# Kernel optimization log

Measured on AMD Instinct MI355X. Metric: run time of the kernel, lower is better.

## Reference

```python
import jax, jax.numpy as jnp
import numpy as np

B, S, W = 64, 128, 20
VOCAB, E, H = 256, 64, 256


def setup_inputs() -> dict:
    key = jax.random.key(0)
    ks = jax.random.split(key, 10)
    return {
        "chars": jax.random.randint(ks[0], (B, S, W), 0, VOCAB),
        "emb": jax.random.uniform(ks[1], (VOCAB, E), jnp.float32, -0.32, 0.32),
        "w1": jax.random.normal(ks[2], (H, E, 1), jnp.float32) * 0.1,
        "b1": jax.random.normal(ks[3], (H,), jnp.float32) * 0.1,
        "w3": jax.random.normal(ks[4], (H, E, 3), jnp.float32) * 0.1,
        "b3": jax.random.normal(ks[5], (H,), jnp.float32) * 0.1,
        "w5": jax.random.normal(ks[6], (H, E, 5), jnp.float32) * 0.1,
        "b5": jax.random.normal(ks[7], (H,), jnp.float32) * 0.1,
        "lw": jax.random.normal(ks[8], (H, 3 * H), jnp.float32) * 0.05,
        "lb": jax.random.normal(ks[9], (H,), jnp.float32) * 0.05,
    }


def _conv_relu_maxpool(x, w, b):
    # x: [N, E, W], w: [H, E, k] ('same' padding k//2) -> [N, H]
    k = w.shape[-1]
    pad = k // 2
    y = jax.lax.conv_general_dilated(
        x, w, window_strides=(1,), padding=[(pad, pad)],
        dimension_numbers=("NCH", "OIH", "NCH"))
    y = jax.nn.relu(y + b[None, :, None])
    return jnp.max(y, axis=2)  # global max over char positions


def reference(chars, emb, w1, b1, w3, b3, w5, b5, lw, lb):
    b, s, wlen = chars.shape
    flat = chars.reshape(-1, wlen)                 # [N, W]
    x = emb[flat]                                  # [N, W, E]
    x = jnp.transpose(x, (0, 2, 1))                # [N, E, W]
    outs = jnp.concatenate([
        _conv_relu_maxpool(x, w1, b1),
        _conv_relu_maxpool(x, w3, b3),
        _conv_relu_maxpool(x, w5, b5),
    ], axis=1)                                     # [N, 3H]
    out = outs @ lw.T + lb                         # [N, H]
    return out.reshape(b, s, -1)
```

## Files before the change

kernel.cpp:

```cpp
#include <hip/hip_runtime.h>
#include <hip/hip_bf16.h>

#define WW 20
#define NW 8192
#define VOCAB 256
#define EE 64
#define HH 256
#define K3 768
#define NTAP 9
#define UNIT 2304

typedef short bf16x8 __attribute__((ext_vector_type(8)));
typedef float f32x4  __attribute__((ext_vector_type(4)));

__device__ __forceinline__ ushort f2bs(float x) {
    __hip_bfloat16 h = __float2bfloat16(x);
    union { __hip_bfloat16 h; ushort u; } c; c.h = h; return c.u;
}
__device__ __forceinline__ float blo(unsigned u) {
    union { unsigned i; float f; } c; c.i = u << 16; return c.f;
}
__device__ __forceinline__ float bhi(unsigned u) {
    union { unsigned i; float f; } c; c.i = u & 0xffff0000u; return c.f;
}
__device__ __forceinline__ unsigned pack2(float lo, float hi) {
    return (unsigned)f2bs(lo) | ((unsigned)f2bs(hi) << 16);
}

#define SET2(d, w) { d[0] = blo(w); d[1] = bhi(w); }
#define ADD2(d, w) { d[0] += blo(w); d[1] += bhi(w); }
#define MAX2(m, s) { m[0] = fmaxf(m[0], s[0]); m[1] = fmaxf(m[1], s[1]); }


__global__ __launch_bounds__(256) void prep(
        const float* __restrict__ w1,
        const float* __restrict__ w3,
        const float* __restrict__ w5,
        const float* __restrict__ lw,
        float* __restrict__ wTp,
        ushort* __restrict__ lwb) {
    const int bid = blockIdx.x;
    if (bid < 576) {
        int idx = bid * 256 + threadIdx.x;
        int e = idx / UNIT;
        int j = idx - e * UNIT;
        int o  = j / 1152;
        int jh = j - o * 1152;
        int tap, h;
        if (jh < 1024) {
            int c = jh >> 8, q = jh & 255, u = q >> 2, p = q & 3;
            tap = 2*c + (p >> 1);
            h   = o*128 + 2*u + (p & 1);
        } else { tap = 8; h = o*128 + (jh - 1024); }
        float v;
        if (tap == 0)      v = w1[h*EE + e];
        else if (tap <= 3) v = w3[(h*EE + e)*3 + (tap-1)];
        else               v = w5[(h*EE + e)*5 + (tap-4)];
        wTp[idx] = v;
    } else {
        int i = ((bid - 576) * 256 + threadIdx.x) * 4;
        float4 v = *(const float4*)(lw + i);
        ushort4 o4;
        o4.x = f2bs(v.x); o4.y = f2bs(v.y); o4.z = f2bs(v.z); o4.w = f2bs(v.w);
        *(ushort4*)(lwb + i) = o4;
    }
}

__global__ __launch_bounds__(256) void build_tables(
        const float* __restrict__ emb,
        const float* __restrict__ wTp,
        ushort* __restrict__ P3) {
    __shared__ float emb_s[4][EE];
    const int v0 = blockIdx.x * 4;
    const int j  = blockIdx.y * 256 + threadIdx.x;
    const int t  = threadIdx.x;
    emb_s[t >> 6][t & 63] = emb[v0*EE + t];
    __syncthreads();

    float a0 = 0.f, a1 = 0.f, a2 = 0.f, a3 = 0.f;
    const float* wp = wTp + j;
    #pragma unroll 8
    for (int e = 0; e < EE; ++e) {
        float w = wp[e * UNIT];
        a0 += emb_s[0][e] * w; a1 += emb_s[1][e] * w;
        a2 += emb_s[2][e] * w; a3 += emb_s[3][e] * w;
    }
    P3[(size_t)(v0+0)*UNIT + j] = f2bs(a0);
    P3[(size_t)(v0+1)*UNIT + j] = f2bs(a1);
    P3[(size_t)(v0+2)*UNIT + j] = f2bs(a2);
    P3[(size_t)(v0+3)*UNIT + j] = f2bs(a3);
}

__global__ __launch_bounds__(256) void conv_pool(
        const int* __restrict__ chars,
        const ushort* __restrict__ P3,
        const float* __restrict__ b1,
        const float* __restrict__ b3,
        const float* __restrict__ b5,
        ushort* __restrict__ outs) {
    const int tid  = threadIdx.x;
    const int wave = tid >> 6, lane = tid & 63;
    const int n    = blockIdx.x * 2 + (wave >> 1);
    const int o    = wave & 1;

    int cv = chars[n * WW + (lane < WW ? lane : WW - 1)];
    int c[WW];
    #pragma unroll
    for (int j = 0; j < WW; ++j) c[j] = __builtin_amdgcn_readlane(cv, j);

    const ushort* base = P3 + o * 1152;

    float acc3[3][2], acc5[5][2], m1[2], m3[2], m5[2];
    acc3[0][0]=0.f; acc3[0][1]=0.f;
    acc5[0][0]=0.f; acc5[0][1]=0.f; acc5[1][0]=0.f; acc5[1][1]=0.f;
    m1[0]=-1e30f; m1[1]=-1e30f; m3[0]=-1e30f; m3[1]=-1e30f;
    m5[0]=-1e30f; m5[1]=-1e30f;

    uint2 q[2][4]; unsigned t8[2];
    {
        const ushort* p = base + (size_t)c[0] * UNIT;
        #pragma unroll
        for (int i = 0; i < 4; ++i) q[0][i] = *(const uint2*)(p + i*256 + lane*4);
        t8[0] = *(const unsigned*)(p + 1024 + lane*2);
    }

    #pragma unroll
    for (int j = 0; j < WW; ++j) {
        const int cur = j & 1, nxt = cur ^ 1;
        if (j + 1 < WW) {
            const ushort* p = base + (size_t)c[j+1] * UNIT;
            #pragma unroll
            for (int i = 0; i < 4; ++i) q[nxt][i] = *(const uint2*)(p + i*256 + lane*4);
            t8[nxt] = *(const unsigned*)(p + 1024 + lane*2);
        }
        uint2 q0 = q[cur][0], q1 = q[cur][1], q2 = q[cur][2], q3 = q[cur][3];
        unsigned e8 = t8[cur];

        m1[0] = fmaxf(m1[0], blo(q0.x)); m1[1] = fmaxf(m1[1], bhi(q0.x));
        if (j + 1 < WW) SET2(acc3[(j+1)%3], q0.y)
        ADD2(acc3[j%3], q1.x)
        if (j >= 1) { ADD2(acc3[(j-1)%3], q1.y)
                      MAX2(m3, acc3[(j-1)%3]) }
        if (j + 2 < WW) SET2(acc5[(j+2)%5], q2.x)
        if (j + 1 < WW) ADD2(acc5[(j+1)%5], q2.y)
        ADD2(acc5[j%5], q3.x)
        if (j >= 1) ADD2(acc5[(j-1)%5], q3.y)
        if (j >= 2) { ADD2(acc5[(j-2)%5], e8)
                      MAX2(m5, acc5[(j-2)%5]) }
    }
    MAX2(m3, acc3[(WW-1)%3])
    MAX2(m5, acc5[(WW-2)%5])
    MAX2(m5, acc5[(WW-1)%5])

    const int h0 = o*128 + lane*2;
    float2 bb1 = *(const float2*)(b1 + h0);
    float2 bb3 = *(const float2*)(b3 + h0);
    float2 bb5 = *(const float2*)(b5 + h0);
    unsigned* op = (unsigned*)(outs + (size_t)n * K3 + h0);
    op[0*(HH/2)] = pack2(fmaxf(m1[0]+bb1.x, 0.f), fmaxf(m1[1]+bb1.y, 0.f));
    op[1*(HH/2)] = pack2(fmaxf(m3[0]+bb3.x, 0.f), fmaxf(m3[1]+bb3.y, 0.f));
    op[2*(HH/2)] = pack2(fmaxf(m5[0]+bb5.x, 0.f), fmaxf(m5[1]+bb5.y, 0.f));
}

__global__ __launch_bounds__(64) void gemm_out(
        const ushort* __restrict__ outs,
        const ushort* __restrict__ lwb,
        const float* __restrict__ lb,
        float* __restrict__ out) {
    const int lane = threadIdx.x;
    const int m0 = blockIdx.x * 16;
    const int n0 = blockIdx.y * 32;
    const int mrow = lane & 15, quad = lane >> 4;

    f32x4 acc0 = (f32x4){0,0,0,0}, acc1 = (f32x4){0,0,0,0};
    const ushort* ap = outs + (size_t)(m0 + mrow) * K3 + quad * 8;
    const ushort* bp = lwb  + (size_t)(n0 + mrow) * K3 + quad * 8;

    bf16x8 a  = *(const bf16x8*)ap;
    bf16x8 b0 = *(const bf16x8*)bp;
    bf16x8 b1 = *(const bf16x8*)(bp + 16*K3);

    #pragma unroll
    for (int it = 0; it < K3/32; ++it) {
        const int kn = (it + 1 < K3/32) ? (it + 1) * 32 : 0;
        bf16x8 an  = *(const bf16x8*)(ap + kn);
        bf16x8 b0n = *(const bf16x8*)(bp + kn);
        bf16x8 b1n = *(const bf16x8*)(bp + 16*K3 + kn);
        acc0 = __builtin_amdgcn_mfma_f32_16x16x32_bf16(a, b0, acc0, 0, 0, 0);
        acc1 = __builtin_amdgcn_mfma_f32_16x16x32_bf16(a, b1, acc1, 0, 0, 0);
        a = an; b0 = b0n; b1 = b1n;
    }

    #pragma unroll
    for (int nn = 0; nn < 2; ++nn) {
        const f32x4 acc = nn ? acc1 : acc0;
        int ncol = n0 + nn*16 + mrow;
        float lbv = lb[ncol];
        #pragma unroll
        for (int r = 0; r < 4; ++r)
            out[(size_t)(m0 + quad*4 + r)*HH + ncol] = acc[r] + lbv;
    }
}

extern "C" void kernel_launch(void* const* d_in, const int* in_sizes, int n_in,
                              void* d_out, int out_size, void* d_ws, size_t ws_size,
                              hipStream_t stream) {
    const int*   chars = (const int*)d_in[0];
    const float* emb   = (const float*)d_in[1];
    const float* w1    = (const float*)d_in[2];
    const float* b1    = (const float*)d_in[3];
    const float* w3    = (const float*)d_in[4];
    const float* b3    = (const float*)d_in[5];
    const float* w5    = (const float*)d_in[6];
    const float* b5    = (const float*)d_in[7];
    const float* lw    = (const float*)d_in[8];
    const float* lb    = (const float*)d_in[9];

    ushort* P3   = (ushort*)d_ws;
    float*  wTp  = (float*)(P3 + VOCAB * UNIT);
    ushort* outs = (ushort*)(wTp + EE * UNIT);
    ushort* lwb  = outs + (size_t)NW * K3;

    prep<<<768, 256, 0, stream>>>(w1, w3, w5, lw, wTp, lwb);
    build_tables<<<dim3(VOCAB/4, NTAP), 256, 0, stream>>>(emb, wTp, P3);
    conv_pool<<<NW/2, 256, 0, stream>>>(chars, P3, b1, b3, b5, outs);
    gemm_out<<<dim3(NW/16, HH/32), 64, 0, stream>>>(outs, lwb, lb, (float*)d_out);
}
```

Before: 161.4 us.

## Repack per-vocab tap table to per-channel contiguous 10-tap layout

The precomputed embedding-times-weight table is reorganised so that each output channel's nine taps sit contiguously, padded to ten entries, per vocab entry. The conv_pool kernel then does one 16-byte and one 4-byte load per character per thread instead of five scattered loads, and handles one channel per thread with one word per block. Lanes now read 20-byte strided addresses, which may coalesce less well. The table grows from nine to ten taps per channel and the output stores become 2-byte writes.

```diff
diff --git a/kernel.cpp b/kernel.cpp
--- a/kernel.cpp
+++ b/kernel.cpp
@@ -7,8 +7,7 @@
 #define EE 64
 #define HH 256
 #define K3 768
-#define NTAP 9
-#define UNIT 2304
+#define UNIT4 2560
 
 typedef short bf16x8 __attribute__((ext_vector_type(8)));
 typedef float f32x4  __attribute__((ext_vector_type(4)));
@@ -23,13 +22,6 @@
 __device__ __forceinline__ float bhi(unsigned u) {
     union { unsigned i; float f; } c; c.i = u & 0xffff0000u; return c.f;
 }
-__device__ __forceinline__ unsigned pack2(float lo, float hi) {
-    return (unsigned)f2bs(lo) | ((unsigned)f2bs(hi) << 16);
-}
-
-#define SET2(d, w) { d[0] = blo(w); d[1] = bhi(w); }
-#define ADD2(d, w) { d[0] += blo(w); d[1] += bhi(w); }
-#define MAX2(m, s) { m[0] = fmaxf(m[0], s[0]); m[1] = fmaxf(m[1], s[1]); }
 
 
 __global__ __launch_bounds__(256) void prep(
@@ -40,25 +32,19 @@
         float* __restrict__ wTp,
         ushort* __restrict__ lwb) {
     const int bid = blockIdx.x;
-    if (bid < 576) {
+    if (bid < 640) {
         int idx = bid * 256 + threadIdx.x;
-        int e = idx / UNIT;
-        int j = idx - e * UNIT;
-        int o  = j / 1152;
-        int jh = j - o * 1152;
-        int tap, h;
-        if (jh < 1024) {
-            int c = jh >> 8, q = jh & 255, u = q >> 2, p = q & 3;
-            tap = 2*c + (p >> 1);
-            h   = o*128 + 2*u + (p & 1);
-        } else { tap = 8; h = o*128 + (jh - 1024); }
-        float v;
+        int e = idx / UNIT4;
+        int j = idx - e * UNIT4;
+        int h = j / 10;
+        int tap = j - h * 10;
+        float v = 0.f;
         if (tap == 0)      v = w1[h*EE + e];
         else if (tap <= 3) v = w3[(h*EE + e)*3 + (tap-1)];
-        else               v = w5[(h*EE + e)*5 + (tap-4)];
+        else if (tap <= 8) v = w5[(h*EE + e)*5 + (tap-4)];
         wTp[idx] = v;
     } else {
-        int i = ((bid - 576) * 256 + threadIdx.x) * 4;
+        int i = ((bid - 640) * 256 + threadIdx.x) * 4;
         float4 v = *(const float4*)(lw + i);
         ushort4 o4;
         o4.x = f2bs(v.x); o4.y = f2bs(v.y); o4.z = f2bs(v.z); o4.w = f2bs(v.w);
@@ -69,7 +55,7 @@
 __global__ __launch_bounds__(256) void build_tables(
         const float* __restrict__ emb,
         const float* __restrict__ wTp,
-        ushort* __restrict__ P3) {
+        ushort* __restrict__ P4) {
     __shared__ float emb_s[4][EE];
     const int v0 = blockIdx.x * 4;
     const int j  = blockIdx.y * 256 + threadIdx.x;
@@ -81,85 +67,81 @@
     const float* wp = wTp + j;
     #pragma unroll 8
     for (int e = 0; e < EE; ++e) {
-        float w = wp[e * UNIT];
+        float w = wp[e * UNIT4];
         a0 += emb_s[0][e] * w; a1 += emb_s[1][e] * w;
         a2 += emb_s[2][e] * w; a3 += emb_s[3][e] * w;
     }
-    P3[(size_t)(v0+0)*UNIT + j] = f2bs(a0);
-    P3[(size_t)(v0+1)*UNIT + j] = f2bs(a1);
-    P3[(size_t)(v0+2)*UNIT + j] = f2bs(a2);
-    P3[(size_t)(v0+3)*UNIT + j] = f2bs(a3);
+    P4[(size_t)(v0+0)*UNIT4 + j] = f2bs(a0);
+    P4[(size_t)(v0+1)*UNIT4 + j] = f2bs(a1);
+    P4[(size_t)(v0+2)*UNIT4 + j] = f2bs(a2);
+    P4[(size_t)(v0+3)*UNIT4 + j] = f2bs(a3);
 }
 
 __global__ __launch_bounds__(256) void conv_pool(
         const int* __restrict__ chars,
-        const ushort* __restrict__ P3,
+        const ushort* __restrict__ P4,
         const float* __restrict__ b1,
         const float* __restrict__ b3,
         const float* __restrict__ b5,
         ushort* __restrict__ outs) {
     const int tid  = threadIdx.x;
     const int wave = tid >> 6, lane = tid & 63;
-    const int n    = blockIdx.x * 2 + (wave >> 1);
-    const int o    = wave & 1;
+    const int n    = blockIdx.x;
+    const int h    = wave * 64 + lane;
+    const int hb   = h * 20;
 
     int cv = chars[n * WW + (lane < WW ? lane : WW - 1)];
     int c[WW];
     #pragma unroll
     for (int j = 0; j < WW; ++j) c[j] = __builtin_amdgcn_readlane(cv, j);
 
-    const ushort* base = P3 + o * 1152;
-
-    float acc3[3][2], acc5[5][2], m1[2], m3[2], m5[2];
-    acc3[0][0]=0.f; acc3[0][1]=0.f;
-    acc5[0][0]=0.f; acc5[0][1]=0.f; acc5[1][0]=0.f; acc5[1][1]=0.f;
-    m1[0]=-1e30f; m1[1]=-1e30f; m3[0]=-1e30f; m3[1]=-1e30f;
-    m5[0]=-1e30f; m5[1]=-1e30f;
-
-    uint2 q[2][4]; unsigned t8[2];
+    float acc3[3], acc5[5], m1, m3, m5;
+    acc3[0] = 0.f; acc5[0] = 0.f; acc5[1] = 0.f;
+    m1 = -1e30f; m3 = -1e30f; m5 = -1e30f;
+
+    uint4 q[2]; unsigned t8[2];
     {
-        const ushort* p = base + (size_t)c[0] * UNIT;
-        #pragma unroll
-        for (int i = 0; i < 4; ++i) q[0][i] = *(const uint2*)(p + i*256 + lane*4);
-        t8[0] = *(const unsigned*)(p + 1024 + lane*2);
+        const char* p = (const char*)P4 + (size_t)c[0] * 5120;
+        q[0]  = *(const uint4*)(p + hb);
+        t8[0] = *(const unsigned*)(p + hb + 16);
     }
 
     #pragma unroll
     for (int j = 0; j < WW; ++j) {
         const int cur = j & 1, nxt = cur ^ 1;
         if (j + 1 < WW) {
-            const ushort* p = base + (size_t)c[j+1] * UNIT;
-            #pragma unroll
-            for (int i = 0; i < 4; ++i) q[nxt][i] = *(const uint2*)(p + i*256 + lane*4);
-            t8[nxt] = *(const unsigned*)(p + 1024 + lane*2);
+            const char* p = (const char*)P4 + (size_t)c[j+1] * 5120;
+            q[nxt]  = *(const uint4*)(p + hb);
+            t8[nxt] = *(const unsigned*)(p + hb + 16);
         }
-        uint2 q0 = q[cur][0], q1 = q[cur][1], q2 = q[cur][2], q3 = q[cur][3];
-        unsigned e8 = t8[cur];
-
-        m1[0] = fmaxf(m1[0], blo(q0.x)); m1[1] = fmaxf(m1[1], bhi(q0.x));
-        if (j + 1 < WW) SET2(acc3[(j+1)%3], q0.y)
-        ADD2(acc3[j%3], q1.x)
-        if (j >= 1) { ADD2(acc3[(j-1)%3], q1.y)
-                      MAX2(m3, acc3[(j-1)%3]) }
-        if (j + 2 < WW) SET2(acc5[(j+2)%5], q2.x)
-        if (j + 1 < WW) ADD2(acc5[(j+1)%5], q2.y)
-        ADD2(acc5[j%5], q3.x)
-        if (j >= 1) ADD2(acc5[(j-1)%5], q3.y)
-        if (j >= 2) { ADD2(acc5[(j-2)%5], e8)
-                      MAX2(m5, acc5[(j-2)%5]) }
-    }
-    MAX2(m3, acc3[(WW-1)%3])
-    MAX2(m5, acc5[(WW-2)%5])
-    MAX2(m5, acc5[(WW-1)%5])
-
-    const int h0 = o*128 + lane*2;
-    float2 bb1 = *(const float2*)(b1 + h0);
-    float2 bb3 = *(const float2*)(b3 + h0);
-    float2 bb5 = *(const float2*)(b5 + h0);
-    unsigned* op = (unsigned*)(outs + (size_t)n * K3 + h0);
-    op[0*(HH/2)] = pack2(fmaxf(m1[0]+bb1.x, 0.f), fmaxf(m1[1]+bb1.y, 0.f));
-    op[1*(HH/2)] = pack2(fmaxf(m3[0]+bb3.x, 0.f), fmaxf(m3[1]+bb3.y, 0.f));
-    op[2*(HH/2)] = pack2(fmaxf(m5[0]+bb5.x, 0.f), fmaxf(m5[1]+bb5.y, 0.f));
+        uint4 qq = q[cur];
+        float t0 = blo(qq.x), t1 = bhi(qq.x), t2 = blo(qq.y), t3 = bhi(qq.y);
+        float t4 = blo(qq.z), t5 = bhi(qq.z), t6 = blo(qq.w), t7 = bhi(qq.w);
+        float t8v = blo(t8[cur]);
+
+        m1 = fmaxf(m1, t0);
+        if (j + 1 < WW) acc3[(j+1)%3] = t1;
+        acc3[j%3] += t2;
+        if (j >= 1) { acc3[(j-1)%3] += t3;
+                      m3 = fmaxf(m3, acc3[(j-1)%3]); }
+        if (j + 2 < WW) acc5[(j+2)%5] = t4;
+        if (j + 1 < WW) acc5[(j+1)%5] += t5;
+        acc5[j%5] += t6;
+        if (j >= 1) acc5[(j-1)%5] += t7;
+        if (j >= 2) { acc5[(j-2)%5] += t8v;
+                      m5 = fmaxf(m5, acc5[(j-2)%5]); }
+    }
+    m3 = fmaxf(m3, acc3[(WW-1)%3]);
+    m5 = fmaxf(m5, acc5[(WW-2)%5]);
+    m5 = fmaxf(m5, acc5[(WW-1)%5]);
+
+    float v1 = fmaxf(m1 + b1[h], 0.f);
+    float v3 = fmaxf(m3 + b3[h], 0.f);
+    float v5 = fmaxf(m5 + b5[h], 0.f);
+    ushort* op = outs + (size_t)n * K3 + h;
+    op[0*HH] = f2bs(v1);
+    op[1*HH] = f2bs(v3);
+    op[2*HH] = f2bs(v5);
 }
 
 __global__ __launch_bounds__(64) void gemm_out(
@@ -216,13 +198,13 @@
     const float* lw    = (const float*)d_in[8];
     const float* lb    = (const float*)d_in[9];
 
-    ushort* P3   = (ushort*)d_ws;
-    float*  wTp  = (float*)(P3 + VOCAB * UNIT);
-    ushort* outs = (ushort*)(wTp + EE * UNIT);
+    ushort* P4   = (ushort*)d_ws;
+    float*  wTp  = (float*)(P4 + VOCAB * UNIT4);
+    ushort* outs = (ushort*)(wTp + EE * UNIT4);
     ushort* lwb  = outs + (size_t)NW * K3;
 
-    prep<<<768, 256, 0, stream>>>(w1, w3, w5, lw, wTp, lwb);
-    build_tables<<<dim3(VOCAB/4, NTAP), 256, 0, stream>>>(emb, wTp, P3);
-    conv_pool<<<NW/2, 256, 0, stream>>>(chars, P3, b1, b3, b5, outs);
+    prep<<<832, 256, 0, stream>>>(w1, w3, w5, lw, wTp, lwb);
+    build_tables<<<dim3(VOCAB/4, 10), 256, 0, stream>>>(emb, wTp, P4);
+    conv_pool<<<NW, 256, 0, stream>>>(chars, P4, b1, b3, b5, outs);
     gemm_out<<<dim3(NW/16, HH/32), 64, 0, stream>>>(outs, lwb, lb, (float*)d_out);
 }
```

After: 160.5 us. Within noise of the previous version (-0.6%).
